# Kernel tuning notes

Hardware: AMD Instinct MI355X
Metric: run time of the kernel (lower is better)

## Reference

```python
import jax, jax.numpy as jnp
import numpy as np

NUM_HEADS = 12
KEEP_RATE = 0.7
INIT_N = 14 * 14  # 196


def setup_inputs() -> dict:
    key = jax.random.key(0)
    k1, k2, k3, k4 = jax.random.split(key, 4)
    B, N, C = 64, 197, 768
    s = 1.0 / np.sqrt(C)
    return {
        "x": jax.random.normal(k1, (B, N, C), dtype=jnp.float32),
        "qkv_w": jax.random.normal(k2, (3 * C, C), dtype=jnp.float32) * s,
        "proj_w": jax.random.normal(k3, (C, C), dtype=jnp.float32) * s,
        "proj_b": jax.random.normal(k4, (C,), dtype=jnp.float32) * 0.01,
    }


def reference(x, qkv_w, proj_w, proj_b):
    B, N, C = x.shape
    H = NUM_HEADS
    hd = C // H
    scale = hd ** (-0.5)

    # qkv projection (torch Linear: y = x @ W.T), split into q, k, v heads
    qkv = (x @ qkv_w.T).reshape(B, N, 3, H, hd)
    qkv = jnp.transpose(qkv, (2, 0, 3, 1, 4))  # [3, B, H, N, hd]
    q, k, v = qkv[0], qkv[1], qkv[2]

    # explicit (non-flash) attention: attn matrix is needed for cls-row pruning
    attn = jax.nn.softmax(jnp.einsum("bhqd,bhkd->bhqk", q, k) * scale, axis=-1)
    out = jnp.einsum("bhqk,bhkd->bqhd", attn, v).reshape(B, N, C)
    out = out @ proj_w.T + proj_b

    # top-k token pruning via mean cls attention over heads
    left_tokens = int(KEEP_RATE * INIT_N)  # 137
    cls_attn = attn[:, :, 0, 1:].mean(axis=1)  # [B, N-1]
    _, idx = jax.lax.top_k(cls_attn, left_tokens)  # sorted descending, like torch.topk
    index = jnp.broadcast_to(idx[:, :, None], (B, left_tokens, C))
    return (out, index, idx)
```

## Files before the change

### kernel.cpp

```cpp
#include <hip/hip_runtime.h>
#include <math.h>


typedef __attribute__((ext_vector_type(8))) short short8;
typedef __attribute__((ext_vector_type(4))) float f32x4;

constexpr int T_B = 64, T_N = 197, T_C = 768, T_H = 12, T_HD = 64;
constexpr int T_M = T_B * T_N;
constexpr int T_KEEP = 137, T_NTOK = 196;

constexpr size_t OOFF_INDEX = (size_t)T_M * T_C;
constexpr size_t OOFF_IDX   = OOFF_INDEX + (size_t)T_B * T_KEEP * T_C;

constexpr size_t U_XB_AO = 0;
constexpr size_t U_QWB   = 9682944;
constexpr size_t U_PWB   = 11452416;
constexpr size_t U_QB    = 12042240;
constexpr size_t U_KB    = 21725184;
constexpr size_t U_VB    = 31408128;
constexpr size_t WS_FP_BYTE = 82182144ull;

__device__ __forceinline__ float bf2f(short u) {
  return __builtin_bit_cast(float, ((unsigned)(unsigned short)u) << 16);
}
__device__ __forceinline__ unsigned short f2bf(float f) {
  unsigned u = __builtin_bit_cast(unsigned, f);
  return (unsigned short)((u + 0x7fffu + ((u >> 16) & 1u)) >> 16);
}

__global__ __launch_bounds__(256) void cvt_k(const float* __restrict__ in,
                                             unsigned short* __restrict__ outp)
{
  const int i = blockIdx.x * 256 + threadIdx.x;
  const float4 v = ((const float4*)in)[i];
  const unsigned long long pk =
      (unsigned long long)f2bf(v.x) | ((unsigned long long)f2bf(v.y) << 16) |
      ((unsigned long long)f2bf(v.z) << 32) | ((unsigned long long)f2bf(v.w) << 48);
  ((unsigned long long*)outp)[i] = pk;
}

__global__ __launch_bounds__(256) void vzero_k(unsigned short* __restrict__ vtg)
{
  const size_t i = ((size_t)blockIdx.x * 256 + threadIdx.x) * 8;
  *(short8*)(vtg + i) = (short8){0, 0, 0, 0, 0, 0, 0, 0};
}

template<int MODE, int NTN>
__global__ __launch_bounds__(256) void mgemm_k(
    const unsigned short* __restrict__ A, const unsigned short* __restrict__ Bw,
    int M, float* __restrict__ outF, const float* __restrict__ bias,
    unsigned short* __restrict__ oq, unsigned short* __restrict__ ok,
    unsigned short* __restrict__ ov)
{
  __shared__ unsigned short ldsA[3][4096], ldsB[3][4096];
  const int t = threadIdx.x, w = t >> 6, lane = t & 63;
  const int wr = w >> 1, wc = w & 1;

  const int nwg = 99 * NTN;
  int id = blockIdx.x;
  {
    const int q = nwg >> 3, r = nwg & 7;
    const int xcd = id & 7, off = id >> 3;
    id = (xcd < r ? xcd * (q + 1) : r * (q + 1) + (xcd - r) * q) + off;
  }
  const int m0 = (id / NTN) * 128, n0 = (id % NTN) * 128;

  const int row0 = t >> 2,        slot0 = t & 3;
  const int row1 = 64 + (t >> 2);
  const int gs0 = slot0 ^ ((row0 >> 1) & 3);
  const int gs1 = slot0 ^ ((row1 >> 1) & 3);
  int ar0 = m0 + row0; ar0 = ar0 < M ? ar0 : M - 1;
  int ar1 = m0 + row1; ar1 = ar1 < M ? ar1 : M - 1;
  const unsigned short* Ab0 = A + (size_t)ar0 * 768 + gs0 * 8;
  const unsigned short* Ab1 = A + (size_t)ar1 * 768 + gs1 * 8;
  const unsigned short* Bb0 = Bw + (size_t)(n0 + row0) * 768 + gs0 * 8;
  const unsigned short* Bb1 = Bw + (size_t)(n0 + row1) * 768 + gs1 * 8;

  const int gsel = lane >> 4, rsel = lane & 15;
  int offA[4], offB[4];
#pragma unroll
  for (int i = 0; i < 4; i++) {
    const int rowa = wr * 64 + i * 16 + rsel;
    offA[i] = rowa * 32 + ((gsel ^ ((rowa >> 1) & 3)) * 8);
    const int rowb = wc * 64 + i * 16 + rsel;
    offB[i] = rowb * 32 + ((gsel ^ ((rowb >> 1) & 3)) * 8);
  }

  auto stage = [&](int buf, int k0) {
    __builtin_amdgcn_global_load_lds(
        (const __attribute__((address_space(1))) unsigned int*)(Ab0 + k0),
        (__attribute__((address_space(3))) unsigned int*)&ldsA[buf][(size_t)t * 8],
        16, 0, 0);
    __builtin_amdgcn_global_load_lds(
        (const __attribute__((address_space(1))) unsigned int*)(Ab1 + k0),
        (__attribute__((address_space(3))) unsigned int*)&ldsA[buf][(size_t)(256 + t) * 8],
        16, 0, 0);
    __builtin_amdgcn_global_load_lds(
        (const __attribute__((address_space(1))) unsigned int*)(Bb0 + k0),
        (__attribute__((address_space(3))) unsigned int*)&ldsB[buf][(size_t)t * 8],
        16, 0, 0);
    __builtin_amdgcn_global_load_lds(
        (const __attribute__((address_space(1))) unsigned int*)(Bb1 + k0),
        (__attribute__((address_space(3))) unsigned int*)&ldsB[buf][(size_t)(256 + t) * 8],
        16, 0, 0);
  };

  f32x4 acc[4][4];
#pragma unroll
  for (int i = 0; i < 4; i++)
#pragma unroll
    for (int j = 0; j < 4; j++) acc[i][j] = (f32x4){0.f, 0.f, 0.f, 0.f};

  stage(0, 0);
  stage(1, 32);

#pragma unroll
  for (int k = 0; k < 24; ++k) {
    __builtin_amdgcn_sched_barrier(0);
    if (k < 23) asm volatile("s_waitcnt vmcnt(4)\n\ts_barrier" ::: "memory");
    else        asm volatile("s_waitcnt vmcnt(0)\n\ts_barrier" ::: "memory");
    __builtin_amdgcn_sched_barrier(0);

    const int cur = k % 3;
    short8 aF[4], bF[4];
#pragma unroll
    for (int mi = 0; mi < 4; mi++) aF[mi] = *(const short8*)&ldsA[cur][offA[mi]];
#pragma unroll
    for (int ni = 0; ni < 4; ni++) bF[ni] = *(const short8*)&ldsB[cur][offB[ni]];

    if (k + 2 < 24) stage((k + 2) % 3, (k + 2) * 32);

#pragma unroll
    for (int mi = 0; mi < 4; mi++)
#pragma unroll
      for (int ni = 0; ni < 4; ni++)
        acc[mi][ni] = __builtin_amdgcn_mfma_f32_16x16x32_bf16(aF[mi], bF[ni], acc[mi][ni], 0, 0, 0);
  }

  const int colL = lane & 15, rowH = lane >> 4;
#pragma unroll
  for (int mi = 0; mi < 4; mi++) {
#pragma unroll
    for (int r = 0; r < 4; r++) {
      const int gm = m0 + wr * 64 + mi * 16 + rowH * 4 + r;
      if (gm >= M) continue;
      int bb = 0, nn = 0;
      if (MODE == 0) { bb = gm / T_N; nn = gm - bb * T_N; }
#pragma unroll
      for (int ni = 0; ni < 4; ni++) {
        const int gc = n0 + wc * 64 + ni * 16 + colL;
        const float val = acc[mi][ni][r];
        if (MODE == 0) {
          const int part = gc / T_C;
          const int rem = gc - part * T_C;
          const int h = rem >> 6, d = rem & 63;
          if (part == 2) {
            ov[(((size_t)(bb * T_H + h)) * 64 + d) * 224 + nn] = f2bf(val);
          } else {
            unsigned short* dst = part == 0 ? oq : ok;
            dst[(((size_t)(bb * T_H + h)) * T_N + nn) * T_HD + d] = f2bf(val);
          }
        } else {
          outF[(size_t)gm * T_C + gc] = val + bias[gc];
        }
      }
    }
  }
}

__global__ __launch_bounds__(256) void flash3_k(
    const unsigned short* __restrict__ qb, const unsigned short* __restrict__ kb,
    const unsigned short* __restrict__ vtg, unsigned short* __restrict__ ao)
{
  __shared__ unsigned short lds[27456];
  constexpr int KL_U = 0;
  constexpr int PL0  = 12608;

  const int bh = blockIdx.x;
  const int b = bh / T_H, h = bh - b * T_H;
  const int t = threadIdx.x;
  const int w = t >> 6, lane = t & 63;
  const int colL = lane & 15, g4 = lane >> 4;
  const int PL_W = PL0 + w * 3712;
  const short8 z8 = (short8){0, 0, 0, 0, 0, 0, 0, 0};

  {
    const unsigned short* src = kb + (size_t)bh * T_N * 64;
    for (int c = t; c < 1576; c += 256) {
      const int row = c >> 3, s = c & 7;
      const short8 v = *(const short8*)(src + row * 64 + s * 8);
      *(short8*)&lds[KL_U + row * 64 + ((s ^ (row & 7)) * 8)] = v;
    }
  }
  if (lane < 16) {
    unsigned short* p = &lds[PL_W + lane * 232];
    *(short8*)&p[208] = z8; *(short8*)&p[216] = z8;
  }
  __syncthreads();

  const size_t qbase = (size_t)bh * T_N * 64;
  const unsigned short* vb2 = vtg + (size_t)bh * 64 * 224;

  for (int qt = w; qt < 13; qt += 4) {
    int qrow = qt * 16 + colL; if (qrow > 196) qrow = 196;
    const short8 qa0 = *(const short8*)(qb + qbase + (size_t)qrow * 64 + g4 * 8);
    const short8 qa1 = *(const short8*)(qb + qbase + (size_t)qrow * 64 + 32 + g4 * 8);

    f32x4 acc[13];
#pragma unroll
    for (int kt = 0; kt < 13; kt++) acc[kt] = (f32x4){0.f, 0.f, 0.f, 0.f};
#pragma unroll
    for (int kt = 0; kt < 13; kt++) {
      const int krow = kt * 16 + colL;
      const int base = KL_U + krow * 64;
      const short8 k0f = *(const short8*)&lds[base + ((g4 ^ (krow & 7)) * 8)];
      const short8 k1f = *(const short8*)&lds[base + (((4 + g4) ^ (krow & 7)) * 8)];
      acc[kt] = __builtin_amdgcn_mfma_f32_16x16x32_bf16(qa0, k0f, acc[kt], 0, 0, 0);
      acc[kt] = __builtin_amdgcn_mfma_f32_16x16x32_bf16(qa1, k1f, acc[kt], 0, 0, 0);
    }

    float l4[4];
#pragma unroll
    for (int r = 0; r < 4; r++) {
      float sv[13];
      float mx = -1e30f;
#pragma unroll
      for (int kt = 0; kt < 13; kt++) {
        const int col = kt * 16 + colL;
        float s = acc[kt][r] * 0.125f;
        if (col > 196) s = -1e30f;
        sv[kt] = s;
        mx = fmaxf(mx, s);
      }
      mx = fmaxf(mx, __shfl_xor(mx, 1));
      mx = fmaxf(mx, __shfl_xor(mx, 2));
      mx = fmaxf(mx, __shfl_xor(mx, 4));
      mx = fmaxf(mx, __shfl_xor(mx, 8));
      float l = 0.f;
      const int prow = g4 * 4 + r;
#pragma unroll
      for (int kt = 0; kt < 13; kt++) {
        const float p = __expf(sv[kt] - mx);
        l += p;
        lds[PL_W + prow * 232 + kt * 16 + colL] = f2bf(p);
      }
      l += __shfl_xor(l, 1);
      l += __shfl_xor(l, 2);
      l += __shfl_xor(l, 4);
      l += __shfl_xor(l, 8);
      l4[r] = l;
    }

    f32x4 oacc[4];
#pragma unroll
    for (int dt = 0; dt < 4; dt++) oacc[dt] = (f32x4){0.f, 0.f, 0.f, 0.f};
#pragma unroll
    for (int ks = 0; ks < 7; ks++) {
      const short8 pa = *(const short8*)&lds[PL_W + colL * 232 + ks * 32 + g4 * 8];
#pragma unroll
      for (int dt = 0; dt < 4; dt++) {
        const short8 vf = *(const short8*)(vb2 + (size_t)(dt * 16 + colL) * 224 + ks * 32 + g4 * 8);
        oacc[dt] = __builtin_amdgcn_mfma_f32_16x16x32_bf16(pa, vf, oacc[dt], 0, 0, 0);
      }
    }

#pragma unroll
    for (int r = 0; r < 4; r++) {
      const int row = qt * 16 + g4 * 4 + r;
      if (row <= 196) {
        const float invl = 1.f / l4[r];
        unsigned short* op = ao + ((size_t)b * T_N + row) * T_C + h * 64;
#pragma unroll
        for (int dt = 0; dt < 4; dt++)
          op[dt * 16 + colL] = f2bf(oacc[dt][r] * invl);
      }
    }
  }
}

__global__ __launch_bounds__(256) void qcls_k(const float* __restrict__ x,
                                              const float* __restrict__ qkvw,
                                              double* __restrict__ qc)
{
  __shared__ double xr[768];
  const int b = blockIdx.x, t = threadIdx.x;
  if (t < 192) {
    const float4 v = *(const float4*)&x[(size_t)b * T_N * T_C + t * 4];
    xr[t * 4 + 0] = (double)v.x; xr[t * 4 + 1] = (double)v.y;
    xr[t * 4 + 2] = (double)v.z; xr[t * 4 + 3] = (double)v.w;
  }
  __syncthreads();
  const int w = t >> 6, lane = t & 63;
  const int jj0 = blockIdx.y * 4;
  for (int jj = jj0; jj < jj0 + 4; jj++) {
    const int j = jj * 4 + w;
    const float* wr = qkvw + (size_t)j * T_C;
    double a = 0.0;
#pragma unroll
    for (int ci = 0; ci < 12; ci++) a += xr[lane + ci * 64] * (double)wr[lane + ci * 64];
#pragma unroll
    for (int off = 32; off > 0; off >>= 1) a += __shfl_xor(a, off);
    if (lane == 0) qc[(size_t)b * T_C + j] = a;
  }
}

__global__ __launch_bounds__(256) void wtil_k(const double* __restrict__ qc,
                                              const float* __restrict__ qkvw,
                                              double* __restrict__ wt)
{
  __shared__ double ql[64];
  const int bh = blockIdx.x;
  const int b = bh / T_H, h = bh - b * T_H;
  const int t = threadIdx.x;
  if (t < 64) ql[t] = qc[(size_t)b * T_C + h * 64 + t];
  __syncthreads();
  const float* wbase = qkvw + ((size_t)T_C + h * 64) * T_C;
  double a0 = 0.0, a1 = 0.0, a2 = 0.0;
  for (int d = 0; d < 64; d++) {
    const double qd = ql[d];
    const float* wr = wbase + (size_t)d * T_C;
    a0 += qd * (double)wr[t];
    a1 += qd * (double)wr[t + 256];
    a2 += qd * (double)wr[t + 512];
  }
  double* o = wt + (size_t)bh * T_C;
  o[t] = a0; o[t + 256] = a1; o[t + 512] = a2;
}

__global__ __launch_bounds__(256) void clslog_k(const float* __restrict__ x,
                                                const double* __restrict__ wt,
                                                double* __restrict__ lg)
{
  const int b = blockIdx.x;
  const int t = threadIdx.x, w = t >> 6, lane = t & 63;

  double wreg[3][12];
#pragma unroll
  for (int i = 0; i < 3; i++) {
    const double* wb = wt + ((size_t)b * T_H + w * 3 + i) * T_C;
#pragma unroll
    for (int ci = 0; ci < 12; ci++) wreg[i][ci] = wb[lane + ci * 64];
  }

  const int n0 = blockIdx.y * 13;
  for (int nn = 0; nn < 13; nn++) {
    const int n = n0 + nn;
    if (n > 196) break;
    const float* xr = x + ((size_t)b * T_N + n) * T_C;
    double p0 = 0.0, p1 = 0.0, p2 = 0.0;
#pragma unroll
    for (int ci = 0; ci < 12; ci++) {
      const double xv = (double)xr[lane + ci * 64];
      p0 += xv * wreg[0][ci];
      p1 += xv * wreg[1][ci];
      p2 += xv * wreg[2][ci];
    }
    double pv[3] = {p0, p1, p2};
#pragma unroll
    for (int i = 0; i < 3; i++) {
      double sv = pv[i];
#pragma unroll
      for (int off = 32; off > 0; off >>= 1) sv += __shfl_xor(sv, off);
      if (lane == 0) lg[((size_t)b * T_H + w * 3 + i) * T_N + n] = sv * 0.125;
    }
  }
}

__global__ __launch_bounds__(256) void final_k(const double* __restrict__ lg,
                                               float* __restrict__ out)
{
  __shared__ double pm[12][200];
  __shared__ unsigned vals[T_NTOK];
  __shared__ int idxb[T_KEEP];
  const int b = blockIdx.x, t = threadIdx.x, w = t >> 6, lane = t & 63;
#pragma unroll
  for (int i = 0; i < 3; i++) {
    const int h = w * 3 + i;
    const double* L = lg + ((size_t)b * T_H + h) * T_N;
    double v[4]; double mx = -1e300;
#pragma unroll
    for (int t2 = 0; t2 < 4; t2++) {
      const int n = lane + t2 * 64;
      v[t2] = (n < T_N) ? L[n] : -1e300;
      mx = fmax(mx, v[t2]);
    }
#pragma unroll
    for (int off = 32; off > 0; off >>= 1) mx = fmax(mx, __shfl_xor(mx, off));
    double s = 0.0;
#pragma unroll
    for (int t2 = 0; t2 < 4; t2++) {
      const int n = lane + t2 * 64;
      const double e = (n < T_N) ? exp(v[t2] - mx) : 0.0;
      v[t2] = e; s += e;
    }
#pragma unroll
    for (int off = 32; off > 0; off >>= 1) s += __shfl_xor(s, off);
    const double inv = 1.0 / s;
#pragma unroll
    for (int t2 = 0; t2 < 4; t2++) {
      const int n = lane + t2 * 64;
      if (n < T_N) pm[h][n] = v[t2] * inv;
    }
  }
  __syncthreads();
  if (t < T_NTOK) {
    double s = 0.0;
#pragma unroll
    for (int h2 = 0; h2 < 12; h2++) s += pm[h2][t + 1];
    const float f = (float)(s / 12.0);
    vals[t] = __builtin_bit_cast(unsigned, f) & ~7u;
  }
  __syncthreads();
  if (t < T_NTOK) {
    const unsigned v = vals[t];
    int r = 0;
    for (int i2 = 0; i2 < T_NTOK; i2++) {
      const unsigned vi = vals[i2];
      r += ((vi > v) || (vi == v && i2 < t)) ? 1 : 0;
    }
    if (r < T_KEEP) idxb[r] = t;
  }
  __syncthreads();
  if (t < T_KEEP) out[OOFF_IDX + (size_t)b * T_KEEP + t] = (float)idxb[t];
  const size_t basei = OOFF_INDEX + (size_t)b * T_KEEP * T_C;
  for (int pos = t; pos < T_KEEP * T_C; pos += 256) out[basei + pos] = (float)idxb[pos / T_C];
}

extern "C" void kernel_launch(void* const* d_in, const int* in_sizes, int n_in,
                              void* d_out, int out_size, void* d_ws, size_t ws_size,
                              hipStream_t stream)
{
  const float* x     = (const float*)d_in[0];
  const float* qkvw  = (const float*)d_in[1];
  const float* projw = (const float*)d_in[2];
  const float* projb = (const float*)d_in[3];
  float* out = (float*)d_out;

  unsigned short* u = (unsigned short*)d_ws;
  unsigned short* xb   = u + U_XB_AO;
  unsigned short* qwb  = u + U_QWB;
  unsigned short* pwb  = u + U_PWB;
  unsigned short* qb   = u + U_QB;
  unsigned short* kb   = u + U_KB;
  unsigned short* vtg  = u + U_VB;
  unsigned short* ao   = u + U_XB_AO;
  double* dr  = (double*)((char*)d_ws + WS_FP_BYTE);
  double* qc  = dr;
  double* wt  = dr + 49152;
  double* lgb = dr + 49152 + 589824;

  const dim3 blk(256);

  qcls_k<<<dim3(64, 48), blk, 0, stream>>>(x, qkvw, qc);
  wtil_k<<<dim3(768), blk, 0, stream>>>(qc, qkvw, wt);
  clslog_k<<<dim3(64, 16), blk, 0, stream>>>(x, wt, lgb);
  final_k<<<dim3(64), blk, 0, stream>>>(lgb, out);

  cvt_k<<<dim3(9456), blk, 0, stream>>>(x, xb);
  cvt_k<<<dim3(1728), blk, 0, stream>>>(qkvw, qwb);
  cvt_k<<<dim3(576),  blk, 0, stream>>>(projw, pwb);
  vzero_k<<<dim3(5376), blk, 0, stream>>>(vtg);
  mgemm_k<0, 18><<<dim3(99 * 18), blk, 0, stream>>>(xb, qwb, T_M, nullptr, nullptr, qb, kb, vtg);
  flash3_k<<<dim3(768), blk, 0, stream>>>(qb, kb, vtg, ao);
  mgemm_k<1, 6><<<dim3(99 * 6), blk, 0, stream>>>(ao, pwb, T_M, out, projb, nullptr, nullptr, nullptr);
}
```

Baseline: 254.2 us.

## Shrink GEMM M-tile to 64 rows to eliminate padded row tiles

Changes the bf16 MFMA GEMM tile from 128x128 to 64x128, so M=12608 (=197*64) divides exactly and the row clamping and bounds checks can be removed. This doubles the workgroup count for both the QKV and projection GEMMs, which improves load balance across CUs and drops the wasted work on the partial last tile. The cost is lower arithmetic intensity per block, since each B tile is reused over half as many rows, along with more global B traffic. The wait count is adjusted because each stage now issues three loads instead of four.

```diff
diff --git a/kernel.cpp b/kernel.cpp
--- a/kernel.cpp
+++ b/kernel.cpp
@@ -48,52 +48,47 @@
 template<int MODE, int NTN>
 __global__ __launch_bounds__(256) void mgemm_k(
     const unsigned short* __restrict__ A, const unsigned short* __restrict__ Bw,
-    int M, float* __restrict__ outF, const float* __restrict__ bias,
+    float* __restrict__ outF, const float* __restrict__ bias,
     unsigned short* __restrict__ oq, unsigned short* __restrict__ ok,
     unsigned short* __restrict__ ov)
 {
-  __shared__ unsigned short ldsA[3][4096], ldsB[3][4096];
+  __shared__ unsigned short ldsA[3][2048], ldsB[3][4096];
   const int t = threadIdx.x, w = t >> 6, lane = t & 63;
   const int wr = w >> 1, wc = w & 1;
 
-  const int nwg = 99 * NTN;
+  const int nwg = 197 * NTN;
   int id = blockIdx.x;
   {
     const int q = nwg >> 3, r = nwg & 7;
     const int xcd = id & 7, off = id >> 3;
     id = (xcd < r ? xcd * (q + 1) : r * (q + 1) + (xcd - r) * q) + off;
   }
-  const int m0 = (id / NTN) * 128, n0 = (id % NTN) * 128;
-
-  const int row0 = t >> 2,        slot0 = t & 3;
-  const int row1 = 64 + (t >> 2);
-  const int gs0 = slot0 ^ ((row0 >> 1) & 3);
-  const int gs1 = slot0 ^ ((row1 >> 1) & 3);
-  int ar0 = m0 + row0; ar0 = ar0 < M ? ar0 : M - 1;
-  int ar1 = m0 + row1; ar1 = ar1 < M ? ar1 : M - 1;
-  const unsigned short* Ab0 = A + (size_t)ar0 * 768 + gs0 * 8;
-  const unsigned short* Ab1 = A + (size_t)ar1 * 768 + gs1 * 8;
-  const unsigned short* Bb0 = Bw + (size_t)(n0 + row0) * 768 + gs0 * 8;
-  const unsigned short* Bb1 = Bw + (size_t)(n0 + row1) * 768 + gs1 * 8;
+  const int m0 = (id / NTN) * 64, n0 = (id % NTN) * 128;
+
+  const int rowS = t >> 2, slotS = t & 3;
+  const int gsA  = slotS ^ ((rowS >> 1) & 3);
+  const int gsB1 = slotS ^ (((rowS + 64) >> 1) & 3);
+  const unsigned short* Ab  = A + (size_t)(m0 + rowS) * 768 + gsA * 8;
+  const unsigned short* Bb0 = Bw + (size_t)(n0 + rowS) * 768 + gsA * 8;
+  const unsigned short* Bb1 = Bw + (size_t)(n0 + 64 + rowS) * 768 + gsB1 * 8;
 
   const int gsel = lane >> 4, rsel = lane & 15;
-  int offA[4], offB[4];
+  int offA[2], offB[4];
+#pragma unroll
+  for (int i = 0; i < 2; i++) {
+    const int rowa = wr * 32 + i * 16 + rsel;
+    offA[i] = rowa * 32 + ((gsel ^ ((rowa >> 1) & 3)) * 8);
+  }
 #pragma unroll
   for (int i = 0; i < 4; i++) {
-    const int rowa = wr * 64 + i * 16 + rsel;
-    offA[i] = rowa * 32 + ((gsel ^ ((rowa >> 1) & 3)) * 8);
     const int rowb = wc * 64 + i * 16 + rsel;
     offB[i] = rowb * 32 + ((gsel ^ ((rowb >> 1) & 3)) * 8);
   }
 
   auto stage = [&](int buf, int k0) {
     __builtin_amdgcn_global_load_lds(
-        (const __attribute__((address_space(1))) unsigned int*)(Ab0 + k0),
+        (const __attribute__((address_space(1))) unsigned int*)(Ab + k0),
         (__attribute__((address_space(3))) unsigned int*)&ldsA[buf][(size_t)t * 8],
-        16, 0, 0);
-    __builtin_amdgcn_global_load_lds(
-        (const __attribute__((address_space(1))) unsigned int*)(Ab1 + k0),
-        (__attribute__((address_space(3))) unsigned int*)&ldsA[buf][(size_t)(256 + t) * 8],
         16, 0, 0);
     __builtin_amdgcn_global_load_lds(
         (const __attribute__((address_space(1))) unsigned int*)(Bb0 + k0),
@@ -105,9 +100,9 @@
         16, 0, 0);
   };
 
-  f32x4 acc[4][4];
-#pragma unroll
-  for (int i = 0; i < 4; i++)
+  f32x4 acc[2][4];
+#pragma unroll
+  for (int i = 0; i < 2; i++)
 #pragma unroll
     for (int j = 0; j < 4; j++) acc[i][j] = (f32x4){0.f, 0.f, 0.f, 0.f};
 
@@ -117,21 +112,21 @@
 #pragma unroll
   for (int k = 0; k < 24; ++k) {
     __builtin_amdgcn_sched_barrier(0);
-    if (k < 23) asm volatile("s_waitcnt vmcnt(4)\n\ts_barrier" ::: "memory");
+    if (k < 23) asm volatile("s_waitcnt vmcnt(3)\n\ts_barrier" ::: "memory");
     else        asm volatile("s_waitcnt vmcnt(0)\n\ts_barrier" ::: "memory");
     __builtin_amdgcn_sched_barrier(0);
 
     const int cur = k % 3;
-    short8 aF[4], bF[4];
-#pragma unroll
-    for (int mi = 0; mi < 4; mi++) aF[mi] = *(const short8*)&ldsA[cur][offA[mi]];
+    short8 aF[2], bF[4];
+#pragma unroll
+    for (int mi = 0; mi < 2; mi++) aF[mi] = *(const short8*)&ldsA[cur][offA[mi]];
 #pragma unroll
     for (int ni = 0; ni < 4; ni++) bF[ni] = *(const short8*)&ldsB[cur][offB[ni]];
 
     if (k + 2 < 24) stage((k + 2) % 3, (k + 2) * 32);
 
 #pragma unroll
-    for (int mi = 0; mi < 4; mi++)
+    for (int mi = 0; mi < 2; mi++)
 #pragma unroll
       for (int ni = 0; ni < 4; ni++)
         acc[mi][ni] = __builtin_amdgcn_mfma_f32_16x16x32_bf16(aF[mi], bF[ni], acc[mi][ni], 0, 0, 0);
@@ -139,11 +134,10 @@
 
   const int colL = lane & 15, rowH = lane >> 4;
 #pragma unroll
-  for (int mi = 0; mi < 4; mi++) {
+  for (int mi = 0; mi < 2; mi++) {
 #pragma unroll
     for (int r = 0; r < 4; r++) {
-      const int gm = m0 + wr * 64 + mi * 16 + rowH * 4 + r;
-      if (gm >= M) continue;
+      const int gm = m0 + wr * 32 + mi * 16 + rowH * 4 + r;
       int bb = 0, nn = 0;
       if (MODE == 0) { bb = gm / T_N; nn = gm - bb * T_N; }
 #pragma unroll
@@ -460,7 +454,7 @@
   cvt_k<<<dim3(1728), blk, 0, stream>>>(qkvw, qwb);
   cvt_k<<<dim3(576),  blk, 0, stream>>>(projw, pwb);
   vzero_k<<<dim3(5376), blk, 0, stream>>>(vtg);
-  mgemm_k<0, 18><<<dim3(99 * 18), blk, 0, stream>>>(xb, qwb, T_M, nullptr, nullptr, qb, kb, vtg);
+  mgemm_k<0, 18><<<dim3(197 * 18), blk, 0, stream>>>(xb, qwb, nullptr, nullptr, qb, kb, vtg);
   flash3_k<<<dim3(768), blk, 0, stream>>>(qb, kb, vtg, ao);
-  mgemm_k<1, 6><<<dim3(99 * 6), blk, 0, stream>>>(ao, pwb, T_M, out, projb, nullptr, nullptr, nullptr);
-}
+  mgemm_k<1, 6><<<dim3(197 * 6), blk, 0, stream>>>(ao, pwb, out, projb, nullptr, nullptr, nullptr);
+}
```

Measured after the change: 268.5 us. 5.6% more time.
